# Kernel optimization log

Hardware: AMD Instinct MI355X
Metric: run time of the kernel (lower is better)

Reference implementation:

```python
import jax, jax.numpy as jnp
import numpy as np

D_OUT = 64  # out_embed_size, also the softmax scale base

def setup_inputs() -> dict:
    key = jax.random.key(0)
    kx, kk, kq, kv = jax.random.split(key, 4)
    B, T, C = 8, 2048, 768
    x = jax.random.normal(kx, (B, T, C), dtype=jnp.float32)
    # torch Linear weights are [out, in]; store as [in, out] for x @ W
    s = 1.0 / np.sqrt(C)
    Wk = jax.random.uniform(kk, (C, D_OUT), jnp.float32, -s, s)
    Wq = jax.random.uniform(kq, (C, D_OUT), jnp.float32, -s, s)
    Wv = jax.random.uniform(kv, (C, D_OUT), jnp.float32, -s, s)
    return {"x": x, "Wq": Wq, "Wk": Wk, "Wv": Wv}

def reference(x, Wq, Wk, Wv):
    B, T, C = x.shape
    q = x @ Wq  # [B,T,D]
    k = x @ Wk
    v = x @ Wv
    scale = D_OUT ** -0.5
    qk = jnp.einsum('btd,bsd->bts', q, k) * scale  # [B,T,T]
    causal = jnp.tril(jnp.ones((T, T), dtype=bool))
    qk = jnp.where(causal, qk, -jnp.inf)
    attn = jax.nn.softmax(qk, axis=-1)
    # dropout p=0.0 -> identity
    return jnp.einsum('bts,bsd->btd', attn, v)
```

## Files before the change

kernel.cpp:

```cpp
#include <hip/hip_runtime.h>
#include <hip/hip_bf16.h>

#define BB 8
#define TT 2048
#define CC 768
#define DD 64
#define BT (BB * TT)

typedef __attribute__((ext_vector_type(8))) short bf16x8;
typedef __attribute__((ext_vector_type(4))) float f32x4;

__device__ __forceinline__ unsigned short f2b(float f) {
  unsigned u = __builtin_bit_cast(unsigned, f);
  u += 0x7fffu + ((u >> 16) & 1u);
  return (unsigned short)(u >> 16);
}

__device__ __forceinline__ bf16x8 pack8(float4 a, float4 b) {
  unsigned short t[8] = {f2b(a.x), f2b(a.y), f2b(a.z), f2b(a.w),
                         f2b(b.x), f2b(b.y), f2b(b.z), f2b(b.w)};
  return *reinterpret_cast<bf16x8*>(t);
}

__device__ __forceinline__ void gl16(const void* g, void* l) {
  __builtin_amdgcn_global_load_lds(
      (const __attribute__((address_space(1))) unsigned int*)g,
      (__attribute__((address_space(3))) unsigned int*)l, 16, 0, 0);
}

#define RAW_BAR()                                \
  do {                                           \
    asm volatile("" ::: "memory");               \
    __builtin_amdgcn_s_barrier();                \
    asm volatile("" ::: "memory");               \
  } while (0)

__global__ __launch_bounds__(256) void wt_kernel(const float* __restrict__ Wq,
                                                 const float* __restrict__ Wk,
                                                 const float* __restrict__ Wv,
                                                 unsigned short* __restrict__ wt) {
  int tid = blockIdx.x * 256 + threadIdx.x;
  if (tid >= 192 * 96) return;
  int k0 = (tid % 96) * 8;
  int c = tid / 96;
  const float* W = (c < 64) ? Wq : (c < 128 ? Wk : Wv);
  int cc = c & 63;
  unsigned short t[8];
#pragma unroll
  for (int e = 0; e < 8; ++e) t[e] = f2b(W[(k0 + e) * 64 + cc]);
  *reinterpret_cast<bf16x8*>(&wt[c * 768 + k0]) = *reinterpret_cast<bf16x8*>(t);
}

__global__ __launch_bounds__(512, 2) void proj_kernel(const float* __restrict__ x,
                                                      const unsigned short* __restrict__ wt,
                                                      unsigned short* __restrict__ qws,
                                                      unsigned short* __restrict__ kws,
                                                      unsigned short* __restrict__ vtws) {
  __shared__ __align__(16) float xl[2][32 * 64];
  __shared__ __align__(16) unsigned short wl[2][192 * 64];

  const int tid = threadIdx.x;
  const int wv = tid >> 6;
  const int l = tid & 63;
  const int lo = l & 15, hi = l >> 4;
  const int rg = wv & 1;
  const int cq = wv >> 1;
  const int m0 = blockIdx.x * 32;

  const int xrow = tid >> 4;
  const int xcs = ((tid & 15) ^ (xrow & 7)) * 4;
  const float* xsrc = x + (size_t)(m0 + xrow) * 768 + xcs;
  const int xdst = (tid & ~63) * 4;

  f32x4 acc[3];
#pragma unroll
  for (int i = 0; i < 3; ++i) acc[i] = (f32x4){0.f, 0.f, 0.f, 0.f};

  auto stage = [&](int buf, int k0) {
    gl16(xsrc + k0, &xl[buf][xdst]);
#pragma unroll
    for (int it = 0; it < 3; ++it) {
      int ch = tid + it * 512;
      int row = ch >> 3;
      int c = ((ch & 7) ^ (row & 7)) * 8;
      gl16(wt + row * 768 + k0 + c, &wl[buf][(ch & ~63) * 8]);
    }
  };

  stage(0, 0);

  const int arow = rg * 16 + lo;
  const int ax = arow & 7;
  int buf = 0;
  for (int step = 0; step < 12; ++step) {
    if (step < 11) {
      stage(buf ^ 1, (step + 1) * 64);
      asm volatile("s_waitcnt vmcnt(4)" ::: "memory");
    } else {
      asm volatile("s_waitcnt vmcnt(0)" ::: "memory");
    }
    __builtin_amdgcn_s_barrier();
    __builtin_amdgcn_sched_barrier(0);

    const float* xb = xl[buf];
    const unsigned short* wb = wl[buf];
    float4 a0 = *reinterpret_cast<const float4*>(&xb[arow * 64 + ((hi * 2 + 0) ^ ax) * 4]);
    float4 a1 = *reinterpret_cast<const float4*>(&xb[arow * 64 + ((hi * 2 + 1) ^ ax) * 4]);
    float4 a2 = *reinterpret_cast<const float4*>(&xb[arow * 64 + ((8 + hi * 2 + 0) ^ ax) * 4]);
    float4 a3 = *reinterpret_cast<const float4*>(&xb[arow * 64 + ((8 + hi * 2 + 1) ^ ax) * 4]);
    bf16x8 af0 = pack8(a0, a1);
    bf16x8 af1 = pack8(a2, a3);
    __builtin_amdgcn_s_setprio(1);
#pragma unroll
    for (int ct = 0; ct < 3; ++ct) {
      int cr = cq * 48 + ct * 16 + lo;
      int cx = cr & 7;
      bf16x8 b0 = *reinterpret_cast<const bf16x8*>(&wb[cr * 64 + ((hi) ^ cx) * 8]);
      bf16x8 b1 = *reinterpret_cast<const bf16x8*>(&wb[cr * 64 + ((4 + hi) ^ cx) * 8]);
      acc[ct] = __builtin_amdgcn_mfma_f32_16x16x32_bf16(af0, b0, acc[ct], 0, 0, 0);
      acc[ct] = __builtin_amdgcn_mfma_f32_16x16x32_bf16(af1, b1, acc[ct], 0, 0, 0);
    }
    __builtin_amdgcn_s_setprio(0);
    RAW_BAR();
    buf ^= 1;
  }

  const float QS = 0.125f * 1.4426950408889634f;
#pragma unroll
  for (int ct = 0; ct < 3; ++ct) {
    const int c = cq * 48 + ct * 16 + lo;
    const int mat = c >> 6;
    const int cc = c & 63;
#pragma unroll
    for (int r = 0; r < 4; ++r) {
      const int m = m0 + rg * 16 + hi * 4 + r;
      float val = acc[ct][r];
      if (mat == 0) {
        qws[m * 64 + cc] = f2b(val * QS);
      } else if (mat == 1) {
        kws[m * 64 + cc] = f2b(val);
      } else {
        vtws[(size_t)((m >> 11) * 64 + cc) * 2048 + (m & 2047)] = f2b(val);
      }
    }
  }
}

__global__ __launch_bounds__(256, 2) void attn_kernel(const unsigned short* __restrict__ qws,
                                                      const unsigned short* __restrict__ kws,
                                                      const unsigned short* __restrict__ vtws,
                                                      float* __restrict__ out) {
  __shared__ __align__(16) unsigned short Kl[2][128 * 64];
  __shared__ __align__(16) unsigned short Vl[2][64 * 128];
  __shared__ __align__(16) unsigned short Pl[4][16 * 40];
  __shared__ float Obuf[2][16][68];
  __shared__ float Ssum[2][16];

  const int tid = threadIdx.x;
  const int s = tid >> 6;
  const int l = tid & 63;
  const int lo = l & 15, hi = l >> 4;
  const int b = blockIdx.x & 7;
  const int u0 = blockIdx.x >> 3;

  const int uA = u0, uB = 127 - u0;
  const int t0A = uA * 16, t0B = uB * 16;
  const int ntA = (uA >> 3) + 1;
  const int ntot = 17;

  const unsigned short* qb = qws + (size_t)b * TT * DD;
  const unsigned short* kb = kws + (size_t)b * TT * DD;
  const unsigned short* vb = vtws + (size_t)b * DD * TT;
  unsigned short* Plw = &Pl[s][0];

  for (int i = tid; i < 2 * 16 * 68; i += 256) (&Obuf[0][0][0])[i] = 0.f;
  if (tid < 32) (&Ssum[0][0])[tid] = 0.f;

  const bf16x8 qA0 = *reinterpret_cast<const bf16x8*>(&qb[(t0A + lo) * 64 + hi * 8]);
  const bf16x8 qA1 = *reinterpret_cast<const bf16x8*>(&qb[(t0A + lo) * 64 + 32 + hi * 8]);
  const bf16x8 qB0 = *reinterpret_cast<const bf16x8*>(&qb[(t0B + lo) * 64 + hi * 8]);
  const bf16x8 qB1 = *reinterpret_cast<const bf16x8*>(&qb[(t0B + lo) * 64 + 32 + hi * 8]);

  auto stage = [&](int buf, int kv0) {
#pragma unroll
    for (int it = 0; it < 4; ++it) {
      int ch = tid + it * 256;
      int kr = ch >> 3;
      int kc = ((ch & 7) ^ (kr & 7)) * 8;
      gl16(kb + (size_t)(kv0 + kr) * 64 + kc, &Kl[buf][(ch & ~63) * 8]);
      int vd = ch >> 4;
      int vc = ((ch & 15) ^ (vd & 7)) * 8;
      gl16(vb + (size_t)vd * 2048 + kv0 + vc, &Vl[buf][(ch & ~63) * 8]);
    }
  };

  f32x4 Oa[4];
#pragma unroll
  for (int n = 0; n < 4; ++n) Oa[n] = (f32x4){0.f, 0.f, 0.f, 0.f};
  float srow[4] = {0.f, 0.f, 0.f, 0.f};

  stage(0, 0);

  int buf = 0;
  for (int j = 0; j < ntot; ++j) {
    if (j + 1 < ntot) {
      const int jn = j + 1;
      stage(buf ^ 1, (jn < ntA ? jn : jn - ntA) * 128);
      asm volatile("s_waitcnt vmcnt(8)" ::: "memory");
    } else {
      asm volatile("s_waitcnt vmcnt(0)" ::: "memory");
    }
    __builtin_amdgcn_s_barrier();
    __builtin_amdgcn_sched_barrier(0);

    const unsigned short* Kb = &Kl[buf][0];
    const unsigned short* Vb = &Vl[buf][0];
    const bool isA = (j < ntA);
    const int t0 = isA ? t0A : t0B;
    const bf16x8 qf0 = isA ? qA0 : qB0;
    const bf16x8 qf1 = isA ? qA1 : qB1;

    f32x4 S0 = (f32x4){0.f, 0.f, 0.f, 0.f};
    f32x4 S1 = (f32x4){0.f, 0.f, 0.f, 0.f};
    __builtin_amdgcn_s_setprio(1);
    {
      int key = s * 32 + lo;
      int kx = key & 7;
      bf16x8 k0f = *reinterpret_cast<const bf16x8*>(&Kb[key * 64 + ((hi) ^ kx) * 8]);
      bf16x8 k1f = *reinterpret_cast<const bf16x8*>(&Kb[key * 64 + ((4 + hi) ^ kx) * 8]);
      S0 = __builtin_amdgcn_mfma_f32_16x16x32_bf16(qf0, k0f, S0, 0, 0, 0);
      S0 = __builtin_amdgcn_mfma_f32_16x16x32_bf16(qf1, k1f, S0, 0, 0, 0);
    }
    {
      int key = s * 32 + 16 + lo;
      int kx = key & 7;
      bf16x8 k0f = *reinterpret_cast<const bf16x8*>(&Kb[key * 64 + ((hi) ^ kx) * 8]);
      bf16x8 k1f = *reinterpret_cast<const bf16x8*>(&Kb[key * 64 + ((4 + hi) ^ kx) * 8]);
      S1 = __builtin_amdgcn_mfma_f32_16x16x32_bf16(qf0, k0f, S1, 0, 0, 0);
      S1 = __builtin_amdgcn_mfma_f32_16x16x32_bf16(qf1, k1f, S1, 0, 0, 0);
    }
    __builtin_amdgcn_s_setprio(0);

    if (j == ntA - 1 || j == ntot - 1) {
      const int kg0 = (isA ? j : j - ntA) * 128 + s * 32 + lo;
#pragma unroll
      for (int r = 0; r < 4; ++r) {
        int qg = t0 + hi * 4 + r;
        if (kg0 > qg) S0[r] = -1e30f;
        if (kg0 + 16 > qg) S1[r] = -1e30f;
      }
    }

#pragma unroll
    for (int r = 0; r < 4; ++r) {
      float p0 = exp2f(S0[r]);
      float p1 = exp2f(S1[r]);
      srow[r] += p0 + p1;
      Plw[(hi * 4 + r) * 40 + lo] = f2b(p0);
      Plw[(hi * 4 + r) * 40 + 16 + lo] = f2b(p1);
    }
    bf16x8 pa = *reinterpret_cast<const bf16x8*>(&Plw[lo * 40 + hi * 8]);

    __builtin_amdgcn_s_setprio(1);
#pragma unroll
    for (int n = 0; n < 4; ++n) {
      int d = n * 16 + lo;
      int dx = d & 7;
      bf16x8 vf = *reinterpret_cast<const bf16x8*>(&Vb[d * 128 + ((s * 4 + hi) ^ dx) * 8]);
      Oa[n] = __builtin_amdgcn_mfma_f32_16x16x32_bf16(pa, vf, Oa[n], 0, 0, 0);
    }
    __builtin_amdgcn_s_setprio(0);

    if (j == ntA - 1) {
#pragma unroll
      for (int n = 0; n < 4; ++n)
#pragma unroll
        for (int r = 0; r < 4; ++r)
          atomicAdd(&Obuf[0][hi * 4 + r][n * 16 + lo], Oa[n][r]);
#pragma unroll
      for (int r = 0; r < 4; ++r) {
        float v = srow[r];
        v += __shfl_xor(v, 1);
        v += __shfl_xor(v, 2);
        v += __shfl_xor(v, 4);
        v += __shfl_xor(v, 8);
        if (lo == 0) atomicAdd(&Ssum[0][hi * 4 + r], v);
        srow[r] = 0.f;
      }
#pragma unroll
      for (int n = 0; n < 4; ++n) Oa[n] = (f32x4){0.f, 0.f, 0.f, 0.f};
    }

    RAW_BAR();
    buf ^= 1;
  }

#pragma unroll
  for (int n = 0; n < 4; ++n)
#pragma unroll
    for (int r = 0; r < 4; ++r)
      atomicAdd(&Obuf[1][hi * 4 + r][n * 16 + lo], Oa[n][r]);
#pragma unroll
  for (int r = 0; r < 4; ++r) {
    float v = srow[r];
    v += __shfl_xor(v, 1);
    v += __shfl_xor(v, 2);
    v += __shfl_xor(v, 4);
    v += __shfl_xor(v, 8);
    if (lo == 0) atomicAdd(&Ssum[1][hi * 4 + r], v);
  }
  __syncthreads();

  {
    const int row = tid >> 4;
    const int c4 = (tid & 15) * 4;
#pragma unroll
    for (int t = 0; t < 2; ++t) {
      const int t0 = t ? t0B : t0A;
      const float inv = 1.0f / Ssum[t][row];
      float4 o;
      o.x = Obuf[t][row][c4 + 0] * inv;
      o.y = Obuf[t][row][c4 + 1] * inv;
      o.z = Obuf[t][row][c4 + 2] * inv;
      o.w = Obuf[t][row][c4 + 3] * inv;
      *reinterpret_cast<float4*>(&out[((size_t)b * TT + t0 + row) * 64 + c4]) = o;
    }
  }
}

extern "C" void kernel_launch(void* const* d_in, const int* in_sizes, int n_in,
                              void* d_out, int out_size, void* d_ws, size_t ws_size,
                              hipStream_t stream) {
  const float* x = (const float*)d_in[0];
  const float* Wq = (const float*)d_in[1];
  const float* Wk = (const float*)d_in[2];
  const float* Wv = (const float*)d_in[3];
  float* out = (float*)d_out;

  char* ws = (char*)d_ws;
  unsigned short* qws = (unsigned short*)(ws);
  unsigned short* kws = (unsigned short*)(ws + (size_t)2 * 1024 * 1024);
  unsigned short* vtws = (unsigned short*)(ws + (size_t)4 * 1024 * 1024);
  unsigned short* wt = (unsigned short*)(ws + (size_t)6 * 1024 * 1024);

  hipLaunchKernelGGL(wt_kernel, dim3(72), dim3(256), 0, stream, Wq, Wk, Wv, wt);
  hipLaunchKernelGGL(proj_kernel, dim3(BT / 32), dim3(512), 0, stream, x, wt, qws, kws, vtws);
  hipLaunchKernelGGL(attn_kernel, dim3(512), dim3(256), 0, stream, qws, kws, vtws, out);
}
```

Baseline: 145.2 us.

## Give each wave its own query rows and drop cross-wave LDS reduction

The attention kernel changes its work split. Before, four waves shared one 16-row query tile split over keys, with paired A/B tiles for load balance, and merged partials through LDS atomics. Now each block owns 64 query rows, each wave computes a full 128-key tile for its own 16 rows and writes its output directly. This removes the atomic reductions and the final syncthreads, but halves the grid to 256 blocks. It also drops the head/tail pairing, so blocks near the end of the sequence do far more iterations than early ones, which risks load imbalance and lower occupancy.

```diff
diff --git a/kernel.cpp b/kernel.cpp
--- a/kernel.cpp
+++ b/kernel.cpp
@@ -146,40 +146,30 @@
   }
 }
 
-__global__ __launch_bounds__(256, 2) void attn_kernel(const unsigned short* __restrict__ qws,
-                                                      const unsigned short* __restrict__ kws,
-                                                      const unsigned short* __restrict__ vtws,
-                                                      float* __restrict__ out) {
+__global__ __launch_bounds__(256) void attn_kernel(const unsigned short* __restrict__ qws,
+                                                   const unsigned short* __restrict__ kws,
+                                                   const unsigned short* __restrict__ vtws,
+                                                   float* __restrict__ out) {
   __shared__ __align__(16) unsigned short Kl[2][128 * 64];
   __shared__ __align__(16) unsigned short Vl[2][64 * 128];
-  __shared__ __align__(16) unsigned short Pl[4][16 * 40];
-  __shared__ float Obuf[2][16][68];
-  __shared__ float Ssum[2][16];
+  __shared__ __align__(16) unsigned short Pl[4][16 * 140];
 
   const int tid = threadIdx.x;
-  const int s = tid >> 6;
+  const int wv = tid >> 6;
   const int l = tid & 63;
   const int lo = l & 15, hi = l >> 4;
   const int b = blockIdx.x & 7;
-  const int u0 = blockIdx.x >> 3;
-
-  const int uA = u0, uB = 127 - u0;
-  const int t0A = uA * 16, t0B = uB * 16;
-  const int ntA = (uA >> 3) + 1;
-  const int ntot = 17;
+  const int u = blockIdx.x >> 3;
+  const int t0 = u * 64 + wv * 16;
+  const int nt = (u >> 1) + 1;
 
   const unsigned short* qb = qws + (size_t)b * TT * DD;
   const unsigned short* kb = kws + (size_t)b * TT * DD;
   const unsigned short* vb = vtws + (size_t)b * DD * TT;
-  unsigned short* Plw = &Pl[s][0];
-
-  for (int i = tid; i < 2 * 16 * 68; i += 256) (&Obuf[0][0][0])[i] = 0.f;
-  if (tid < 32) (&Ssum[0][0])[tid] = 0.f;
-
-  const bf16x8 qA0 = *reinterpret_cast<const bf16x8*>(&qb[(t0A + lo) * 64 + hi * 8]);
-  const bf16x8 qA1 = *reinterpret_cast<const bf16x8*>(&qb[(t0A + lo) * 64 + 32 + hi * 8]);
-  const bf16x8 qB0 = *reinterpret_cast<const bf16x8*>(&qb[(t0B + lo) * 64 + hi * 8]);
-  const bf16x8 qB1 = *reinterpret_cast<const bf16x8*>(&qb[(t0B + lo) * 64 + 32 + hi * 8]);
+  unsigned short* Plw = &Pl[wv][0];
+
+  const bf16x8 qf0 = *reinterpret_cast<const bf16x8*>(&qb[(t0 + lo) * 64 + hi * 8]);
+  const bf16x8 qf1 = *reinterpret_cast<const bf16x8*>(&qb[(t0 + lo) * 64 + 32 + hi * 8]);
 
   auto stage = [&](int buf, int kv0) {
 #pragma unroll
@@ -196,16 +186,16 @@
 
   f32x4 Oa[4];
 #pragma unroll
-  for (int n = 0; n < 4; ++n) Oa[n] = (f32x4){0.f, 0.f, 0.f, 0.f};
+  for (int m = 0; m < 4; ++m) Oa[m] = (f32x4){0.f, 0.f, 0.f, 0.f};
   float srow[4] = {0.f, 0.f, 0.f, 0.f};
 
   stage(0, 0);
 
+  const int kx = lo & 7;
   int buf = 0;
-  for (int j = 0; j < ntot; ++j) {
-    if (j + 1 < ntot) {
-      const int jn = j + 1;
-      stage(buf ^ 1, (jn < ntA ? jn : jn - ntA) * 128);
+  for (int j = 0; j < nt; ++j) {
+    if (j + 1 < nt) {
+      stage(buf ^ 1, (j + 1) * 128);
       asm volatile("s_waitcnt vmcnt(8)" ::: "memory");
     } else {
       asm volatile("s_waitcnt vmcnt(0)" ::: "memory");
@@ -215,91 +205,65 @@
 
     const unsigned short* Kb = &Kl[buf][0];
     const unsigned short* Vb = &Vl[buf][0];
-    const bool isA = (j < ntA);
-    const int t0 = isA ? t0A : t0B;
-    const bf16x8 qf0 = isA ? qA0 : qB0;
-    const bf16x8 qf1 = isA ? qA1 : qB1;
-
-    f32x4 S0 = (f32x4){0.f, 0.f, 0.f, 0.f};
-    f32x4 S1 = (f32x4){0.f, 0.f, 0.f, 0.f};
+
+    f32x4 S[8];
     __builtin_amdgcn_s_setprio(1);
-    {
-      int key = s * 32 + lo;
-      int kx = key & 7;
+#pragma unroll
+    for (int n = 0; n < 8; ++n) {
+      const int key = n * 16 + lo;
       bf16x8 k0f = *reinterpret_cast<const bf16x8*>(&Kb[key * 64 + ((hi) ^ kx) * 8]);
       bf16x8 k1f = *reinterpret_cast<const bf16x8*>(&Kb[key * 64 + ((4 + hi) ^ kx) * 8]);
-      S0 = __builtin_amdgcn_mfma_f32_16x16x32_bf16(qf0, k0f, S0, 0, 0, 0);
-      S0 = __builtin_amdgcn_mfma_f32_16x16x32_bf16(qf1, k1f, S0, 0, 0, 0);
-    }
-    {
-      int key = s * 32 + 16 + lo;
-      int kx = key & 7;
-      bf16x8 k0f = *reinterpret_cast<const bf16x8*>(&Kb[key * 64 + ((hi) ^ kx) * 8]);
-      bf16x8 k1f = *reinterpret_cast<const bf16x8*>(&Kb[key * 64 + ((4 + hi) ^ kx) * 8]);
-      S1 = __builtin_amdgcn_mfma_f32_16x16x32_bf16(qf0, k0f, S1, 0, 0, 0);
-      S1 = __builtin_amdgcn_mfma_f32_16x16x32_bf16(qf1, k1f, S1, 0, 0, 0);
+      S[n] = (f32x4){0.f, 0.f, 0.f, 0.f};
+      S[n] = __builtin_amdgcn_mfma_f32_16x16x32_bf16(qf0, k0f, S[n], 0, 0, 0);
+      S[n] = __builtin_amdgcn_mfma_f32_16x16x32_bf16(qf1, k1f, S[n], 0, 0, 0);
     }
     __builtin_amdgcn_s_setprio(0);
 
-    if (j == ntA - 1 || j == ntot - 1) {
-      const int kg0 = (isA ? j : j - ntA) * 128 + s * 32 + lo;
+    if (j == nt - 1) {
+#pragma unroll
+      for (int n = 0; n < 8; ++n) {
+        const int kg = j * 128 + n * 16 + lo;
+#pragma unroll
+        for (int r = 0; r < 4; ++r) {
+          if (kg > t0 + hi * 4 + r) S[n][r] = -1e30f;
+        }
+      }
+    }
+
+#pragma unroll
+    for (int n = 0; n < 8; ++n)
 #pragma unroll
       for (int r = 0; r < 4; ++r) {
-        int qg = t0 + hi * 4 + r;
-        if (kg0 > qg) S0[r] = -1e30f;
-        if (kg0 + 16 > qg) S1[r] = -1e30f;
+        float p = exp2f(S[n][r]);
+        srow[r] += p;
+        Plw[(hi * 4 + r) * 140 + n * 16 + lo] = f2b(p);
       }
-    }
-
-#pragma unroll
-    for (int r = 0; r < 4; ++r) {
-      float p0 = exp2f(S0[r]);
-      float p1 = exp2f(S1[r]);
-      srow[r] += p0 + p1;
-      Plw[(hi * 4 + r) * 40 + lo] = f2b(p0);
-      Plw[(hi * 4 + r) * 40 + 16 + lo] = f2b(p1);
-    }
-    bf16x8 pa = *reinterpret_cast<const bf16x8*>(&Plw[lo * 40 + hi * 8]);
+
+    bf16x8 pa0 = *reinterpret_cast<const bf16x8*>(&Plw[lo * 140 + hi * 8]);
+    bf16x8 pa1 = *reinterpret_cast<const bf16x8*>(&Plw[lo * 140 + 32 + hi * 8]);
+    bf16x8 pa2 = *reinterpret_cast<const bf16x8*>(&Plw[lo * 140 + 64 + hi * 8]);
+    bf16x8 pa3 = *reinterpret_cast<const bf16x8*>(&Plw[lo * 140 + 96 + hi * 8]);
 
     __builtin_amdgcn_s_setprio(1);
 #pragma unroll
-    for (int n = 0; n < 4; ++n) {
-      int d = n * 16 + lo;
-      int dx = d & 7;
-      bf16x8 vf = *reinterpret_cast<const bf16x8*>(&Vb[d * 128 + ((s * 4 + hi) ^ dx) * 8]);
-      Oa[n] = __builtin_amdgcn_mfma_f32_16x16x32_bf16(pa, vf, Oa[n], 0, 0, 0);
+    for (int m = 0; m < 4; ++m) {
+      const int d = m * 16 + lo;
+      const int dx = d & 7;
+      bf16x8 v0 = *reinterpret_cast<const bf16x8*>(&Vb[d * 128 + ((hi + 0) ^ dx) * 8]);
+      bf16x8 v1 = *reinterpret_cast<const bf16x8*>(&Vb[d * 128 + ((hi + 4) ^ dx) * 8]);
+      bf16x8 v2 = *reinterpret_cast<const bf16x8*>(&Vb[d * 128 + ((hi + 8) ^ dx) * 8]);
+      bf16x8 v3 = *reinterpret_cast<const bf16x8*>(&Vb[d * 128 + ((hi + 12) ^ dx) * 8]);
+      Oa[m] = __builtin_amdgcn_mfma_f32_16x16x32_bf16(pa0, v0, Oa[m], 0, 0, 0);
+      Oa[m] = __builtin_amdgcn_mfma_f32_16x16x32_bf16(pa1, v1, Oa[m], 0, 0, 0);
+      Oa[m] = __builtin_amdgcn_mfma_f32_16x16x32_bf16(pa2, v2, Oa[m], 0, 0, 0);
+      Oa[m] = __builtin_amdgcn_mfma_f32_16x16x32_bf16(pa3, v3, Oa[m], 0, 0, 0);
     }
     __builtin_amdgcn_s_setprio(0);
-
-    if (j == ntA - 1) {
-#pragma unroll
-      for (int n = 0; n < 4; ++n)
-#pragma unroll
-        for (int r = 0; r < 4; ++r)
-          atomicAdd(&Obuf[0][hi * 4 + r][n * 16 + lo], Oa[n][r]);
-#pragma unroll
-      for (int r = 0; r < 4; ++r) {
-        float v = srow[r];
-        v += __shfl_xor(v, 1);
-        v += __shfl_xor(v, 2);
-        v += __shfl_xor(v, 4);
-        v += __shfl_xor(v, 8);
-        if (lo == 0) atomicAdd(&Ssum[0][hi * 4 + r], v);
-        srow[r] = 0.f;
-      }
-#pragma unroll
-      for (int n = 0; n < 4; ++n) Oa[n] = (f32x4){0.f, 0.f, 0.f, 0.f};
-    }
 
     RAW_BAR();
     buf ^= 1;
   }
 
-#pragma unroll
-  for (int n = 0; n < 4; ++n)
-#pragma unroll
-    for (int r = 0; r < 4; ++r)
-      atomicAdd(&Obuf[1][hi * 4 + r][n * 16 + lo], Oa[n][r]);
 #pragma unroll
   for (int r = 0; r < 4; ++r) {
     float v = srow[r];
@@ -307,25 +271,15 @@
     v += __shfl_xor(v, 2);
     v += __shfl_xor(v, 4);
     v += __shfl_xor(v, 8);
-    if (lo == 0) atomicAdd(&Ssum[1][hi * 4 + r], v);
+    srow[r] = 1.0f / v;
   }
-  __syncthreads();
-
-  {
-    const int row = tid >> 4;
-    const int c4 = (tid & 15) * 4;
-#pragma unroll
-    for (int t = 0; t < 2; ++t) {
-      const int t0 = t ? t0B : t0A;
-      const float inv = 1.0f / Ssum[t][row];
-      float4 o;
-      o.x = Obuf[t][row][c4 + 0] * inv;
-      o.y = Obuf[t][row][c4 + 1] * inv;
-      o.z = Obuf[t][row][c4 + 2] * inv;
-      o.w = Obuf[t][row][c4 + 3] * inv;
-      *reinterpret_cast<float4*>(&out[((size_t)b * TT + t0 + row) * 64 + c4]) = o;
-    }
-  }
+
+  float* ob = out + ((size_t)b * TT + t0) * 64;
+#pragma unroll
+  for (int m = 0; m < 4; ++m)
+#pragma unroll
+    for (int r = 0; r < 4; ++r)
+      ob[(hi * 4 + r) * 64 + m * 16 + lo] = Oa[m][r] * srow[r];
 }
 
 extern "C" void kernel_launch(void* const* d_in, const int* in_sizes, int n_in,
@@ -345,5 +299,5 @@
 
   hipLaunchKernelGGL(wt_kernel, dim3(72), dim3(256), 0, stream, Wq, Wk, Wv, wt);
   hipLaunchKernelGGL(proj_kernel, dim3(BT / 32), dim3(512), 0, stream, x, wt, qws, kws, vtws);
-  hipLaunchKernelGGL(attn_kernel, dim3(512), dim3(256), 0, stream, qws, kws, vtws, out);
-}
+  hipLaunchKernelGGL(attn_kernel, dim3(256), dim3(256), 0, stream, qws, kws, vtws, out);
+}
```

Result: no change. 143.8 us (-1.0%).
